# Optimization experiments

Hardware: AMD Instinct MI355X
Metric: run time of the kernel (lower is better)

The kernel has to match this reference:

```python
import jax, jax.numpy as jnp
import numpy as np

LN_EPS = 1e-5

def setup_inputs() -> dict:
    key = jax.random.key(0)
    ks = jax.random.split(key, 5)
    B, S, Dv, Dl, V = 4, 576, 1024, 4096, 32000
    return {
        "vision_feats": jax.random.normal(ks[0], (B, S, Dv), dtype=jnp.float32),
        "W1_w": jax.random.normal(ks[1], (Dl, Dv), dtype=jnp.float32) * (Dv ** -0.5),
        "W1_b": jax.random.normal(ks[2], (Dl,), dtype=jnp.float32) * 0.02,
        "W2_w": jax.random.normal(ks[3], (V, Dl), dtype=jnp.float32) * (Dl ** -0.5),
        "llm_token_embed": jax.random.normal(ks[4], (V, Dl), dtype=jnp.float32) * 0.02,
    }

def reference(vision_feats, W1_w, W1_b, W2_w, llm_token_embed):
    # W1: (B,S,Dv) @ (Dv,Dl) + b -> (B,S,Dl)
    x = jnp.einsum('bsd,ed->bse', vision_feats, W1_w) + W1_b
    # layer_norm over last dim, no affine params
    mu = jnp.mean(x, axis=-1, keepdims=True)
    var = jnp.mean(jnp.square(x - mu), axis=-1, keepdims=True)
    xn = (x - mu) * jax.lax.rsqrt(var + LN_EPS)
    # W2 (no bias): (B,S,Dl) -> (B,S,V) vocab logits
    logits = jnp.einsum('bse,ve->bsv', xn, W2_w)
    P = jax.nn.softmax(logits, axis=-1)
    # softmax-weighted mixture of LLM token embeddings: (B,S,V) @ (V,Dl)
    F_align = jnp.einsum('bsv,ve->bse', P, llm_token_embed)
    return F_align
```

## Files before the change

kernel.cpp:

```cpp
#include <hip/hip_runtime.h>
#include <hip/hip_bf16.h>
#include <stdint.h>

typedef __bf16 bf16_t;
typedef __attribute__((ext_vector_type(8))) __bf16 bf16x8;
typedef __attribute__((ext_vector_type(4))) __bf16 bf16x4;
typedef __attribute__((ext_vector_type(4))) float f32x4;
typedef __attribute__((ext_vector_type(8))) unsigned short u16x8;

#define M_TOK 2304
#define DV    1024
#define DLAT  4096
#define VOCAB 32000

__device__ __forceinline__ float bf2f(unsigned short u) {
  union { unsigned int i; float f; } v; v.i = ((unsigned int)u) << 16; return v.f;
}
__device__ __forceinline__ bf16_t f2bf(float f) { return (bf16_t)f; }

#define GLOAD16(gp, lp) \
  __builtin_amdgcn_global_load_lds( \
      (const __attribute__((address_space(1))) unsigned int*)(const void*)(gp), \
      (__attribute__((address_space(3))) unsigned int*)(void*)(lp), 16, 0, 0)

template<int BN_, int WM_, int WN_, int EPI, int MINW>
__global__ void __launch_bounds__(512, MINW)
gemm256(const bf16_t* __restrict__ Ap, const bf16_t* __restrict__ Bp,
        void* __restrict__ Cp0, void* __restrict__ Cp1,
        int Ksplit, int ld, int ldc, int Mt, int Nt)
{
  constexpr int WMR = 256 / WM_;
  constexpr int NFM = WMR / 16;
  constexpr int NFN = (BN_ / WN_) / 16;
  constexpr int PM  = NFM / 4;
  constexpr int BLOADS = BN_ / 128;
  constexpr int L = 2 + BLOADS;

  __shared__ __align__(16) bf16_t Al[3][256 * 32];
  __shared__ __align__(16) bf16_t Bl[3][BN_ * 32];

  const int nwg = gridDim.x;
  const int orig = blockIdx.x;
  const int q = nwg >> 3, r = nwg & 7;
  const int xcd = orig & 7, idx = orig >> 3;
  const int wg = (xcd < r ? xcd * (q + 1) : r * (q + 1) + (xcd - r) * q) + idx;
  const int mt = wg % Mt;
  const int nt = (wg / Mt) % Nt;
  const int sp = wg / (Mt * Nt);
  const int m0 = mt * 256, n0 = nt * BN_;
  const int kb0 = sp * Ksplit;

  const int t    = threadIdx.x;
  const int lane = t & 63, wv = t >> 6;
  const int wm = wv / WN_, wn = wv % WN_;
  const int lr = lane & 15, kc = lane >> 4;

  const int rql = lane >> 2;
  const int cbs = (((lane & 3) ^ ((lane >> 3) & 3)) * 16);
  const int sw8 = (kc ^ ((lr >> 1) & 3)) * 8;
  const size_t rstride = (size_t)ld * 2;

  f32x4 acc[NFM][NFN];
#pragma unroll
  for (int i = 0; i < NFM; ++i)
#pragma unroll
    for (int j = 0; j < NFN; ++j)
#pragma unroll
      for (int x = 0; x < 4; ++x) acc[i][j][x] = 0.0f;

  const int NT = Ksplit / 32;

  auto SG = [&](int kt, int nb, int which) {
    const size_t kb = (size_t)(kb0 + kt * 32) * 2;
    if (which < 2) {
      const char* g = (const char*)Ap + (size_t)(m0 + wv * 32 + rql) * rstride
                      + (size_t)which * 16 * rstride + kb + cbs;
      char* l = (char*)&Al[nb][0] + wv * 2048 + which * 1024;
      GLOAD16(g, l);
    } else if (BLOADS == 2) {
      const int w2 = which - 2;
      const char* g = (const char*)Bp + (size_t)(n0 + wv * 32 + rql) * rstride
                      + (size_t)w2 * 16 * rstride + kb + cbs;
      char* l = (char*)&Bl[nb][0] + wv * 2048 + w2 * 1024;
      GLOAD16(g, l);
    } else {
      const char* g = (const char*)Bp + (size_t)(n0 + wv * 16 + rql) * rstride + kb + cbs;
      char* l = (char*)&Bl[nb][0] + wv * 1024;
      GLOAD16(g, l);
    }
  };

  auto TILE = [&](int bc, int bs, int kt, int stg, int wait) {
    bf16x8 bfv[NFN];
#pragma unroll
    for (int p = 0; p < 4; ++p) {
      bf16x8 af[PM];
      if (p == 0) {
#pragma unroll
        for (int g = 0; g < NFN; ++g)
          bfv[g] = *(const bf16x8*)(&Bl[bc][(wn * 64 + g * 16 + lr) * 32 + sw8]);
      }
#pragma unroll
      for (int s = 0; s < PM; ++s)
        af[s] = *(const bf16x8*)(&Al[bc][(wm * WMR + (p * PM + s) * 16 + lr) * 32 + sw8]);
      if (stg) {
        if (p < 2) SG(kt + 2, bs, p);
        else if (p - 2 < BLOADS) SG(kt + 2, bs, p);
      }
      if (p == 3) {
        if (wait == 1) {
          if constexpr (L == 4) asm volatile("s_waitcnt vmcnt(4)" ::: "memory");
          else                  asm volatile("s_waitcnt vmcnt(3)" ::: "memory");
        } else if (wait == 2) {
          asm volatile("s_waitcnt vmcnt(0)" ::: "memory");
        }
      }
      __builtin_amdgcn_s_barrier();
      __builtin_amdgcn_s_setprio(1);
#pragma unroll
      for (int s = 0; s < PM; ++s)
#pragma unroll
        for (int g = 0; g < NFN; ++g)
          acc[p * PM + s][g] =
            __builtin_amdgcn_mfma_f32_16x16x32_bf16(af[s], bfv[g], acc[p * PM + s][g], 0, 0, 0);
      __builtin_amdgcn_s_setprio(0);
    }
  };

#pragma unroll
  for (int w = 0; w < L; ++w) SG(0, 0, w);
#pragma unroll
  for (int w = 0; w < L; ++w) SG(1, 1, w);
  if constexpr (L == 4) asm volatile("s_waitcnt vmcnt(4)" ::: "memory");
  else                  asm volatile("s_waitcnt vmcnt(3)" ::: "memory");
  __builtin_amdgcn_s_barrier();

  int c0 = 0, c1 = 1, c2 = 2;
  int kt = 0;
  for (; kt < NT - 2; ++kt) {
    TILE(c0, c2, kt, 1, 1);
    const int tmp = c0; c0 = c1; c1 = c2; c2 = tmp;
  }
  TILE(c0, c2, kt, 0, 2);
  { const int tmp = c0; c0 = c1; c1 = c2; c2 = tmp; }
  TILE(c0, c2, kt + 1, 0, 0);

  float* Cf = (EPI == 2) ? (sp == 0 ? (float*)Cp0 : (float*)Cp1) : (float*)Cp0;
#pragma unroll
  for (int j = 0; j < NFN; ++j) {
    const int col = n0 + wn * 64 + j * 16 + lr;
#pragma unroll
    for (int i = 0; i < NFM; ++i) {
      const int row = m0 + wm * WMR + i * 16 + kc * 4;
      f32x4 a4 = acc[i][j];
      if (EPI == 1) {
        bf16_t* C = (bf16_t*)Cp0;
#pragma unroll
        for (int x = 0; x < 4; ++x) C[(size_t)(row + x) * ldc + col] = f2bf(a4[x]);
      } else {
#pragma unroll
        for (int x = 0; x < 4; ++x) Cf[(size_t)(row + x) * ldc + col] = a4[x];
      }
    }
  }
}

constexpr int GBM = 128, GBN = 128, GBK = 32;

template<int EPI>
__global__ void __launch_bounds__(256, 3)
gemm_bb(const bf16_t* __restrict__ Ap, const bf16_t* __restrict__ Bp,
        void* __restrict__ Cp, const float* __restrict__ bias,
        int K, int ldc, int Mt)
{
  __shared__ __align__(16) bf16_t Al[3][GBM * GBK];
  __shared__ __align__(16) bf16_t Bl[3][GBN * GBK];

  const int nwg = gridDim.x;
  const int orig = blockIdx.x;
  const int q = nwg >> 3, r = nwg & 7;
  const int xcd = orig & 7, idx = orig >> 3;
  const int wg = (xcd < r ? xcd * (q + 1) : r * (q + 1) + (xcd - r) * q) + idx;
  const int mt = wg % Mt, nt = wg / Mt;
  const int m0 = mt * GBM, n0 = nt * GBN;

  const int t    = threadIdx.x;
  const int lane = t & 63, wv = t >> 6;
  const int wm = wv >> 1, wn = wv & 1;
  const int lr = lane & 15, kc = lane >> 4;

  f32x4 acc[4][4];
#pragma unroll
  for (int i = 0; i < 4; ++i)
#pragma unroll
    for (int j = 0; j < 4; ++j)
#pragma unroll
      for (int x = 0; x < 4; ++x) acc[i][j][x] = 0.0f;

  const int rql = lane >> 2;
  const int cbs = (((lane & 3) ^ ((lane >> 3) & 3)) * 16);
  const int sw8 = (kc ^ ((lr >> 1) & 3)) * 8;
  const size_t rstride = (size_t)K * 2;

  const int NT = K / GBK;

  auto STAGE = [&](int kt, int nb) {
    const size_t kb = (size_t)kt * GBK * 2;
    const char* ga = (const char*)Ap + (size_t)(m0 + wv * 32 + rql) * rstride + kb + cbs;
    char* la = (char*)&Al[nb][0] + wv * 2048;
    GLOAD16(ga, la);
    GLOAD16(ga + 16 * rstride, la + 1024);
    const char* gb = (const char*)Bp + (size_t)(n0 + wv * 32 + rql) * rstride + kb + cbs;
    char* lb = (char*)&Bl[nb][0] + wv * 2048;
    GLOAD16(gb, lb);
    GLOAD16(gb + 16 * rstride, lb + 1024);
  };

  auto COMPUTE = [&](int nb) {
    bf16x8 af[4], bfv[4];
#pragma unroll
    for (int f = 0; f < 4; ++f)
      af[f] = *(const bf16x8*)(&Al[nb][(wm * 64 + f * 16 + lr) * GBK + sw8]);
#pragma unroll
    for (int f = 0; f < 4; ++f)
      bfv[f] = *(const bf16x8*)(&Bl[nb][(wn * 64 + f * 16 + lr) * GBK + sw8]);
    __builtin_amdgcn_s_setprio(1);
#pragma unroll
    for (int i = 0; i < 4; ++i)
#pragma unroll
      for (int j = 0; j < 4; ++j)
        acc[i][j] = __builtin_amdgcn_mfma_f32_16x16x32_bf16(af[i], bfv[j], acc[i][j], 0, 0, 0);
    __builtin_amdgcn_s_setprio(0);
  };

  auto BARX = [&]() {
    asm volatile("s_waitcnt lgkmcnt(0)" ::: "memory");
    __builtin_amdgcn_s_barrier();
  };

  STAGE(0, 0);
  STAGE(1, 1);
  asm volatile("s_waitcnt vmcnt(4)" ::: "memory");
  __builtin_amdgcn_s_barrier();

  int bc = 0, bn = 1, bs = 2;
  for (int kt = 0; kt < NT - 2; ++kt) {
    STAGE(kt + 2, bs);
    COMPUTE(bc);
    asm volatile("s_waitcnt vmcnt(4)" ::: "memory");
    BARX();
    const int tmp = bc; bc = bn; bn = bs; bs = tmp;
  }
  COMPUTE(bc);
  asm volatile("s_waitcnt vmcnt(0)" ::: "memory");
  BARX();
  COMPUTE(bn);

#pragma unroll
  for (int j = 0; j < 4; ++j) {
    const int col = n0 + wn * 64 + j * 16 + lr;
    float bv = 0.0f;
    if (EPI == 0) bv = bias[col];
#pragma unroll
    for (int i = 0; i < 4; ++i) {
      const int row = m0 + wm * 64 + i * 16 + kc * 4;
      f32x4 a4 = acc[i][j];
      if (EPI == 1) {
        bf16_t* C = (bf16_t*)Cp;
#pragma unroll
        for (int x = 0; x < 4; ++x) C[(size_t)(row + x) * ldc + col] = f2bf(a4[x]);
      } else {
        float* C = (float*)Cp;
#pragma unroll
        for (int x = 0; x < 4; ++x) C[(size_t)(row + x) * ldc + col] = a4[x] + bv;
      }
    }
  }
}

__global__ void __launch_bounds__(256)
addk(float* __restrict__ out, const float* __restrict__ part, int n4)
{
  const int stride = gridDim.x * 256;
  for (int i = blockIdx.x * 256 + threadIdx.x; i < n4; i += stride) {
    f32x4 a = *(const f32x4*)(out + i * 4);
    f32x4 b = *(const f32x4*)(part + i * 4);
#pragma unroll
    for (int x = 0; x < 4; ++x) a[x] += b[x];
    *(f32x4*)(out + i * 4) = a;
  }
}

__global__ void __launch_bounds__(256)
cvt_bf16_k(const float* __restrict__ in, bf16_t* __restrict__ out, long n8)
{
  const long stride = (long)gridDim.x * 256;
  for (long i = (long)blockIdx.x * 256 + threadIdx.x; i < n8; i += stride) {
    f32x4 a = *(const f32x4*)(in + i * 8);
    f32x4 b = *(const f32x4*)(in + i * 8 + 4);
    bf16x8 o;
#pragma unroll
    for (int j = 0; j < 4; ++j) { o[j] = f2bf(a[j]); o[j + 4] = f2bf(b[j]); }
    *(bf16x8*)(out + i * 8) = o;
  }
}

__global__ void __launch_bounds__(256)
embT_k(const float* __restrict__ E, bf16_t* __restrict__ ET)
{
  __shared__ bf16_t tl[64][72];
  const int vb = blockIdx.x % (VOCAB / 64);
  const int eb = blockIdx.x / (VOCAB / 64);
  const int v0 = vb * 64, e0 = eb * 64;
  const int t = threadIdx.x;

  const int rr = t >> 4, c4 = (t & 15) * 4;
#pragma unroll
  for (int p = 0; p < 4; ++p) {
    const float* src = E + (size_t)(v0 + rr + p * 16) * DLAT + e0 + c4;
    f32x4 a = *(const f32x4*)src;
#pragma unroll
    for (int j = 0; j < 4; ++j) tl[c4 + j][rr + p * 16] = f2bf(a[j]);
  }
  __syncthreads();

  const int el = t >> 3, v8 = (t & 7) * 8;
#pragma unroll
  for (int p = 0; p < 2; ++p) {
    bf16x8 o = *(const bf16x8*)(&tl[el + p * 32][v8]);
    *(bf16x8*)(ET + (size_t)(e0 + el + p * 32) * VOCAB + v0 + v8) = o;
  }
}

__global__ void __launch_bounds__(256)
ln_k(const float* __restrict__ x, bf16_t* __restrict__ xn)
{
  __shared__ float sm[4];
  const int row = blockIdx.x, t = threadIdx.x;
  const float* xr = x + (size_t)row * DLAT;
  f32x4 v[4];
#pragma unroll
  for (int i = 0; i < 4; ++i) v[i] = *(const f32x4*)(xr + (t + i * 256) * 4);

  float s = 0.0f;
#pragma unroll
  for (int i = 0; i < 4; ++i)
#pragma unroll
    for (int j = 0; j < 4; ++j) s += v[i][j];
#pragma unroll
  for (int o = 32; o > 0; o >>= 1) s += __shfl_xor(s, o, 64);
  if ((t & 63) == 0) sm[t >> 6] = s;
  __syncthreads();
  const float mean = (sm[0] + sm[1] + sm[2] + sm[3]) * (1.0f / DLAT);
  __syncthreads();

  float qv = 0.0f;
#pragma unroll
  for (int i = 0; i < 4; ++i)
#pragma unroll
    for (int j = 0; j < 4; ++j) { float d = v[i][j] - mean; qv += d * d; }
#pragma unroll
  for (int o = 32; o > 0; o >>= 1) qv += __shfl_xor(qv, o, 64);
  if ((t & 63) == 0) sm[t >> 6] = qv;
  __syncthreads();
  const float varr = (sm[0] + sm[1] + sm[2] + sm[3]) * (1.0f / DLAT);
  const float rs = rsqrtf(varr + 1e-5f);

  bf16_t* outr = xn + (size_t)row * DLAT;
#pragma unroll
  for (int i = 0; i < 4; ++i) {
    bf16x4 o;
#pragma unroll
    for (int j = 0; j < 4; ++j) o[j] = f2bf((v[i][j] - mean) * rs);
    *(bf16x4*)(outr + (t + i * 256) * 4) = o;
  }
}

__global__ void __launch_bounds__(256)
softmax_k(bf16_t* __restrict__ L)
{
  __shared__ __align__(16) bf16_t rs_[VOCAB];
  __shared__ float sm[4];
  const int row = blockIdx.x, t = threadIdx.x;
  bf16_t* lrow = L + (size_t)row * VOCAB;
  const int NF = VOCAB / 8;

  float m = -3.0e38f;
  for (int f = t; f < NF; f += 256) {
    u16x8 u = *(const u16x8*)(&lrow[f * 8]);
    *(u16x8*)(&rs_[f * 8]) = u;
#pragma unroll
    for (int j = 0; j < 8; ++j) m = fmaxf(m, bf2f(u[j]));
  }
#pragma unroll
  for (int o = 32; o > 0; o >>= 1) m = fmaxf(m, __shfl_xor(m, o, 64));
  if ((t & 63) == 0) sm[t >> 6] = m;
  __syncthreads();
  m = fmaxf(fmaxf(sm[0], sm[1]), fmaxf(sm[2], sm[3]));
  __syncthreads();

  float s = 0.0f;
  for (int f = t; f < NF; f += 256) {
    u16x8 u = *(const u16x8*)(&rs_[f * 8]);
#pragma unroll
    for (int j = 0; j < 8; ++j) s += __expf(bf2f(u[j]) - m);
  }
#pragma unroll
  for (int o = 32; o > 0; o >>= 1) s += __shfl_xor(s, o, 64);
  if ((t & 63) == 0) sm[t >> 6] = s;
  __syncthreads();
  const float inv = 1.0f / (sm[0] + sm[1] + sm[2] + sm[3]);

  for (int f = t; f < NF; f += 256) {
    u16x8 u = *(const u16x8*)(&rs_[f * 8]);
    bf16x8 o;
#pragma unroll
    for (int j = 0; j < 8; ++j) o[j] = f2bf(__expf(bf2f(u[j]) - m) * inv);
    *(bf16x8*)(&lrow[f * 8]) = o;
  }
}

extern "C" void kernel_launch(void* const* d_in, const int* in_sizes, int n_in,
                              void* d_out, int out_size, void* d_ws, size_t ws_size,
                              hipStream_t stream)
{
  (void)in_sizes; (void)n_in; (void)out_size; (void)ws_size;
  const float* vision = (const float*)d_in[0];
  const float* W1w    = (const float*)d_in[1];
  const float* W1b    = (const float*)d_in[2];
  const float* W2w    = (const float*)d_in[3];
  const float* Emb    = (const float*)d_in[4];
  float* out = (float*)d_out;

  char* ws = (char*)d_ws;
  bf16_t* xn     = (bf16_t*)ws;
  bf16_t* logits = (bf16_t*)(ws + 18874368);
  float*  xbuf   = (float*)(ws + 166330368);
  bf16_t* wslot  = (bf16_t*)(ws + 204079104);
  bf16_t* xnv    = (bf16_t*)(ws + 466223104);
  bf16_t* w1b    = (bf16_t*)(ws + 470941696);

  cvt_bf16_k<<<dim3(512), dim3(256), 0, stream>>>(vision, xnv, (long)M_TOK * DV / 8);
  cvt_bf16_k<<<dim3(512), dim3(256), 0, stream>>>(W1w, w1b, (long)DLAT * DV / 8);

  gemm_bb<0><<<dim3((M_TOK / GBM) * (DLAT / GBN)), dim3(256), 0, stream>>>(
      xnv, w1b, xbuf, W1b, DV, DLAT, M_TOK / GBM);

  ln_k<<<dim3(M_TOK), dim3(256), 0, stream>>>(xbuf, xn);

  cvt_bf16_k<<<dim3(2048), dim3(256), 0, stream>>>(W2w, wslot, (long)VOCAB * DLAT / 8);

  gemm256<256, 2, 4, 1, 2><<<dim3(9 * 125), dim3(512), 0, stream>>>(
      xn, wslot, logits, nullptr, DLAT, DLAT, VOCAB, 9, 125);

  embT_k<<<dim3((VOCAB / 64) * (DLAT / 64)), dim3(256), 0, stream>>>(Emb, wslot);

  softmax_k<<<dim3(M_TOK), dim3(256), 0, stream>>>(logits);

  gemm256<128, 4, 2, 2, 4><<<dim3(9 * 32 * 2), dim3(512), 0, stream>>>(
      logits, wslot, out, xbuf, VOCAB / 2, VOCAB, DLAT, 9, 32);

  addk<<<dim3(1024), dim3(256), 0, stream>>>(out, xbuf, (M_TOK * DLAT) / 4);
}
```

Before: 2.300 ms.

## Replace 256-row GEMM kernel with templated 128x64 tile GEMM and drop split-K

Removes the 512-thread 256-row gemm256 kernel and generalizes gemm_bb over the N tile width. The two large GEMMs (logits and the embedding mixture) now run on 128x64 tiles with 256 threads. The final GEMM is no longer split along K, so the second partial buffer and the addk reduction kernel go away. The smaller tiles give more workgroups and fewer registers per thread, but each tile reuses less data, so arithmetic intensity drops and more operand traffic goes through L2.

```diff
diff --git a/kernel.cpp b/kernel.cpp
--- a/kernel.cpp
+++ b/kernel.cpp
@@ -23,158 +23,17 @@
       (const __attribute__((address_space(1))) unsigned int*)(const void*)(gp), \
       (__attribute__((address_space(3))) unsigned int*)(void*)(lp), 16, 0, 0)
 
-template<int BN_, int WM_, int WN_, int EPI, int MINW>
-__global__ void __launch_bounds__(512, MINW)
-gemm256(const bf16_t* __restrict__ Ap, const bf16_t* __restrict__ Bp,
-        void* __restrict__ Cp0, void* __restrict__ Cp1,
-        int Ksplit, int ld, int ldc, int Mt, int Nt)
-{
-  constexpr int WMR = 256 / WM_;
-  constexpr int NFM = WMR / 16;
-  constexpr int NFN = (BN_ / WN_) / 16;
-  constexpr int PM  = NFM / 4;
-  constexpr int BLOADS = BN_ / 128;
-  constexpr int L = 2 + BLOADS;
-
-  __shared__ __align__(16) bf16_t Al[3][256 * 32];
-  __shared__ __align__(16) bf16_t Bl[3][BN_ * 32];
-
-  const int nwg = gridDim.x;
-  const int orig = blockIdx.x;
-  const int q = nwg >> 3, r = nwg & 7;
-  const int xcd = orig & 7, idx = orig >> 3;
-  const int wg = (xcd < r ? xcd * (q + 1) : r * (q + 1) + (xcd - r) * q) + idx;
-  const int mt = wg % Mt;
-  const int nt = (wg / Mt) % Nt;
-  const int sp = wg / (Mt * Nt);
-  const int m0 = mt * 256, n0 = nt * BN_;
-  const int kb0 = sp * Ksplit;
-
-  const int t    = threadIdx.x;
-  const int lane = t & 63, wv = t >> 6;
-  const int wm = wv / WN_, wn = wv % WN_;
-  const int lr = lane & 15, kc = lane >> 4;
-
-  const int rql = lane >> 2;
-  const int cbs = (((lane & 3) ^ ((lane >> 3) & 3)) * 16);
-  const int sw8 = (kc ^ ((lr >> 1) & 3)) * 8;
-  const size_t rstride = (size_t)ld * 2;
-
-  f32x4 acc[NFM][NFN];
-#pragma unroll
-  for (int i = 0; i < NFM; ++i)
-#pragma unroll
-    for (int j = 0; j < NFN; ++j)
-#pragma unroll
-      for (int x = 0; x < 4; ++x) acc[i][j][x] = 0.0f;
-
-  const int NT = Ksplit / 32;
-
-  auto SG = [&](int kt, int nb, int which) {
-    const size_t kb = (size_t)(kb0 + kt * 32) * 2;
-    if (which < 2) {
-      const char* g = (const char*)Ap + (size_t)(m0 + wv * 32 + rql) * rstride
-                      + (size_t)which * 16 * rstride + kb + cbs;
-      char* l = (char*)&Al[nb][0] + wv * 2048 + which * 1024;
-      GLOAD16(g, l);
-    } else if (BLOADS == 2) {
-      const int w2 = which - 2;
-      const char* g = (const char*)Bp + (size_t)(n0 + wv * 32 + rql) * rstride
-                      + (size_t)w2 * 16 * rstride + kb + cbs;
-      char* l = (char*)&Bl[nb][0] + wv * 2048 + w2 * 1024;
-      GLOAD16(g, l);
-    } else {
-      const char* g = (const char*)Bp + (size_t)(n0 + wv * 16 + rql) * rstride + kb + cbs;
-      char* l = (char*)&Bl[nb][0] + wv * 1024;
-      GLOAD16(g, l);
-    }
-  };
-
-  auto TILE = [&](int bc, int bs, int kt, int stg, int wait) {
-    bf16x8 bfv[NFN];
-#pragma unroll
-    for (int p = 0; p < 4; ++p) {
-      bf16x8 af[PM];
-      if (p == 0) {
-#pragma unroll
-        for (int g = 0; g < NFN; ++g)
-          bfv[g] = *(const bf16x8*)(&Bl[bc][(wn * 64 + g * 16 + lr) * 32 + sw8]);
-      }
-#pragma unroll
-      for (int s = 0; s < PM; ++s)
-        af[s] = *(const bf16x8*)(&Al[bc][(wm * WMR + (p * PM + s) * 16 + lr) * 32 + sw8]);
-      if (stg) {
-        if (p < 2) SG(kt + 2, bs, p);
-        else if (p - 2 < BLOADS) SG(kt + 2, bs, p);
-      }
-      if (p == 3) {
-        if (wait == 1) {
-          if constexpr (L == 4) asm volatile("s_waitcnt vmcnt(4)" ::: "memory");
-          else                  asm volatile("s_waitcnt vmcnt(3)" ::: "memory");
-        } else if (wait == 2) {
-          asm volatile("s_waitcnt vmcnt(0)" ::: "memory");
-        }
-      }
-      __builtin_amdgcn_s_barrier();
-      __builtin_amdgcn_s_setprio(1);
-#pragma unroll
-      for (int s = 0; s < PM; ++s)
-#pragma unroll
-        for (int g = 0; g < NFN; ++g)
-          acc[p * PM + s][g] =
-            __builtin_amdgcn_mfma_f32_16x16x32_bf16(af[s], bfv[g], acc[p * PM + s][g], 0, 0, 0);
-      __builtin_amdgcn_s_setprio(0);
-    }
-  };
-
-#pragma unroll
-  for (int w = 0; w < L; ++w) SG(0, 0, w);
-#pragma unroll
-  for (int w = 0; w < L; ++w) SG(1, 1, w);
-  if constexpr (L == 4) asm volatile("s_waitcnt vmcnt(4)" ::: "memory");
-  else                  asm volatile("s_waitcnt vmcnt(3)" ::: "memory");
-  __builtin_amdgcn_s_barrier();
-
-  int c0 = 0, c1 = 1, c2 = 2;
-  int kt = 0;
-  for (; kt < NT - 2; ++kt) {
-    TILE(c0, c2, kt, 1, 1);
-    const int tmp = c0; c0 = c1; c1 = c2; c2 = tmp;
-  }
-  TILE(c0, c2, kt, 0, 2);
-  { const int tmp = c0; c0 = c1; c1 = c2; c2 = tmp; }
-  TILE(c0, c2, kt + 1, 0, 0);
-
-  float* Cf = (EPI == 2) ? (sp == 0 ? (float*)Cp0 : (float*)Cp1) : (float*)Cp0;
-#pragma unroll
-  for (int j = 0; j < NFN; ++j) {
-    const int col = n0 + wn * 64 + j * 16 + lr;
-#pragma unroll
-    for (int i = 0; i < NFM; ++i) {
-      const int row = m0 + wm * WMR + i * 16 + kc * 4;
-      f32x4 a4 = acc[i][j];
-      if (EPI == 1) {
-        bf16_t* C = (bf16_t*)Cp0;
-#pragma unroll
-        for (int x = 0; x < 4; ++x) C[(size_t)(row + x) * ldc + col] = f2bf(a4[x]);
-      } else {
-#pragma unroll
-        for (int x = 0; x < 4; ++x) Cf[(size_t)(row + x) * ldc + col] = a4[x];
-      }
-    }
-  }
-}
-
-constexpr int GBM = 128, GBN = 128, GBK = 32;
-
-template<int EPI>
-__global__ void __launch_bounds__(256, 3)
+template<int BN_, int EPI, int MINW>
+__global__ void __launch_bounds__(256, MINW)
 gemm_bb(const bf16_t* __restrict__ Ap, const bf16_t* __restrict__ Bp,
         void* __restrict__ Cp, const float* __restrict__ bias,
         int K, int ldc, int Mt)
 {
-  __shared__ __align__(16) bf16_t Al[3][GBM * GBK];
-  __shared__ __align__(16) bf16_t Bl[3][GBN * GBK];
+  constexpr int NFN = BN_ / 32;
+  constexpr int WNE = BN_ / 2;
+
+  __shared__ __align__(16) bf16_t Al[3][128 * 32];
+  __shared__ __align__(16) bf16_t Bl[3][BN_ * 32];
 
   const int nwg = gridDim.x;
   const int orig = blockIdx.x;
@@ -182,18 +41,18 @@
   const int xcd = orig & 7, idx = orig >> 3;
   const int wg = (xcd < r ? xcd * (q + 1) : r * (q + 1) + (xcd - r) * q) + idx;
   const int mt = wg % Mt, nt = wg / Mt;
-  const int m0 = mt * GBM, n0 = nt * GBN;
+  const int m0 = mt * 128, n0 = nt * BN_;
 
   const int t    = threadIdx.x;
   const int lane = t & 63, wv = t >> 6;
   const int wm = wv >> 1, wn = wv & 1;
   const int lr = lane & 15, kc = lane >> 4;
 
-  f32x4 acc[4][4];
+  f32x4 acc[4][NFN];
 #pragma unroll
   for (int i = 0; i < 4; ++i)
 #pragma unroll
-    for (int j = 0; j < 4; ++j)
+    for (int j = 0; j < NFN; ++j)
 #pragma unroll
       for (int x = 0; x < 4; ++x) acc[i][j][x] = 0.0f;
 
@@ -202,37 +61,47 @@
   const int sw8 = (kc ^ ((lr >> 1) & 3)) * 8;
   const size_t rstride = (size_t)K * 2;
 
-  const int NT = K / GBK;
+  const int NT = K / 32;
 
   auto STAGE = [&](int kt, int nb) {
-    const size_t kb = (size_t)kt * GBK * 2;
+    const size_t kb = (size_t)kt * 64;
     const char* ga = (const char*)Ap + (size_t)(m0 + wv * 32 + rql) * rstride + kb + cbs;
     char* la = (char*)&Al[nb][0] + wv * 2048;
     GLOAD16(ga, la);
     GLOAD16(ga + 16 * rstride, la + 1024);
-    const char* gb = (const char*)Bp + (size_t)(n0 + wv * 32 + rql) * rstride + kb + cbs;
-    char* lb = (char*)&Bl[nb][0] + wv * 2048;
-    GLOAD16(gb, lb);
-    GLOAD16(gb + 16 * rstride, lb + 1024);
+    if constexpr (BN_ == 128) {
+      const char* gb = (const char*)Bp + (size_t)(n0 + wv * 32 + rql) * rstride + kb + cbs;
+      char* lb = (char*)&Bl[nb][0] + wv * 2048;
+      GLOAD16(gb, lb);
+      GLOAD16(gb + 16 * rstride, lb + 1024);
+    } else {
+      const char* gb = (const char*)Bp + (size_t)(n0 + wv * 16 + rql) * rstride + kb + cbs;
+      char* lb = (char*)&Bl[nb][0] + wv * 1024;
+      GLOAD16(gb, lb);
+    }
   };
 
   auto COMPUTE = [&](int nb) {
-    bf16x8 af[4], bfv[4];
+    bf16x8 af[4], bfv[NFN];
 #pragma unroll
     for (int f = 0; f < 4; ++f)
-      af[f] = *(const bf16x8*)(&Al[nb][(wm * 64 + f * 16 + lr) * GBK + sw8]);
-#pragma unroll
-    for (int f = 0; f < 4; ++f)
-      bfv[f] = *(const bf16x8*)(&Bl[nb][(wn * 64 + f * 16 + lr) * GBK + sw8]);
+      af[f] = *(const bf16x8*)(&Al[nb][(wm * 64 + f * 16 + lr) * 32 + sw8]);
+#pragma unroll
+    for (int f = 0; f < NFN; ++f)
+      bfv[f] = *(const bf16x8*)(&Bl[nb][(wn * WNE + f * 16 + lr) * 32 + sw8]);
     __builtin_amdgcn_s_setprio(1);
 #pragma unroll
     for (int i = 0; i < 4; ++i)
 #pragma unroll
-      for (int j = 0; j < 4; ++j)
+      for (int j = 0; j < NFN; ++j)
         acc[i][j] = __builtin_amdgcn_mfma_f32_16x16x32_bf16(af[i], bfv[j], acc[i][j], 0, 0, 0);
     __builtin_amdgcn_s_setprio(0);
   };
 
+  auto WAITL = [&]() {
+    if constexpr (BN_ == 128) asm volatile("s_waitcnt vmcnt(4)" ::: "memory");
+    else                      asm volatile("s_waitcnt vmcnt(3)" ::: "memory");
+  };
   auto BARX = [&]() {
     asm volatile("s_waitcnt lgkmcnt(0)" ::: "memory");
     __builtin_amdgcn_s_barrier();
@@ -240,14 +109,14 @@
 
   STAGE(0, 0);
   STAGE(1, 1);
-  asm volatile("s_waitcnt vmcnt(4)" ::: "memory");
+  WAITL();
   __builtin_amdgcn_s_barrier();
 
   int bc = 0, bn = 1, bs = 2;
   for (int kt = 0; kt < NT - 2; ++kt) {
     STAGE(kt + 2, bs);
     COMPUTE(bc);
-    asm volatile("s_waitcnt vmcnt(4)" ::: "memory");
+    WAITL();
     BARX();
     const int tmp = bc; bc = bn; bn = bs; bs = tmp;
   }
@@ -257,8 +126,8 @@
   COMPUTE(bn);
 
 #pragma unroll
-  for (int j = 0; j < 4; ++j) {
-    const int col = n0 + wn * 64 + j * 16 + lr;
+  for (int j = 0; j < NFN; ++j) {
+    const int col = n0 + wn * WNE + j * 16 + lr;
     float bv = 0.0f;
     if (EPI == 0) bv = bias[col];
 #pragma unroll
@@ -275,19 +144,6 @@
         for (int x = 0; x < 4; ++x) C[(size_t)(row + x) * ldc + col] = a4[x] + bv;
       }
     }
-  }
-}
-
-__global__ void __launch_bounds__(256)
-addk(float* __restrict__ out, const float* __restrict__ part, int n4)
-{
-  const int stride = gridDim.x * 256;
-  for (int i = blockIdx.x * 256 + threadIdx.x; i < n4; i += stride) {
-    f32x4 a = *(const f32x4*)(out + i * 4);
-    f32x4 b = *(const f32x4*)(part + i * 4);
-#pragma unroll
-    for (int x = 0; x < 4; ++x) a[x] += b[x];
-    *(f32x4*)(out + i * 4) = a;
   }
 }
 
@@ -443,22 +299,20 @@
   cvt_bf16_k<<<dim3(512), dim3(256), 0, stream>>>(vision, xnv, (long)M_TOK * DV / 8);
   cvt_bf16_k<<<dim3(512), dim3(256), 0, stream>>>(W1w, w1b, (long)DLAT * DV / 8);
 
-  gemm_bb<0><<<dim3((M_TOK / GBM) * (DLAT / GBN)), dim3(256), 0, stream>>>(
-      xnv, w1b, xbuf, W1b, DV, DLAT, M_TOK / GBM);
+  gemm_bb<128, 0, 3><<<dim3(18 * 32), dim3(256), 0, stream>>>(
+      xnv, w1b, xbuf, W1b, DV, DLAT, 18);
 
   ln_k<<<dim3(M_TOK), dim3(256), 0, stream>>>(xbuf, xn);
 
   cvt_bf16_k<<<dim3(2048), dim3(256), 0, stream>>>(W2w, wslot, (long)VOCAB * DLAT / 8);
 
-  gemm256<256, 2, 4, 1, 2><<<dim3(9 * 125), dim3(512), 0, stream>>>(
-      xn, wslot, logits, nullptr, DLAT, DLAT, VOCAB, 9, 125);
+  gemm_bb<64, 1, 4><<<dim3(18 * 500), dim3(256), 0, stream>>>(
+      xn, wslot, logits, nullptr, DLAT, VOCAB, 18);
 
   embT_k<<<dim3((VOCAB / 64) * (DLAT / 64)), dim3(256), 0, stream>>>(Emb, wslot);
 
   softmax_k<<<dim3(M_TOK), dim3(256), 0, stream>>>(logits);
 
-  gemm256<128, 4, 2, 2, 4><<<dim3(9 * 32 * 2), dim3(512), 0, stream>>>(
-      logits, wslot, out, xbuf, VOCAB / 2, VOCAB, DLAT, 9, 32);
-
-  addk<<<dim3(1024), dim3(256), 0, stream>>>(out, xbuf, (M_TOK * DLAT) / 4);
-}
+  gemm_bb<64, 2, 4><<<dim3(18 * 64), dim3(256), 0, stream>>>(
+      logits, wslot, out, nullptr, VOCAB, DLAT, 18);
+}
```

Result: slower. 2.759 ms (+19.9%).
